# Kernel optimization log

Hardware: AMD Instinct MI355X
Metric: run time of the kernel (lower is better)

## Reference

```python
import jax, jax.numpy as jnp
import numpy as np

EPS = 1e-5  # BatchNorm eps; eval-mode BN with running_mean=0, running_var=1 -> affine


def pe3d(C, x, y, z):
    """PositionalEncoding3D -> (C, x, y, z), faithfully reproducing the torch
    broadcasting (emb_x of shape (x,1,c) assigned into (x,y,z,c) slices)."""
    c = int(np.ceil(C / 3))
    inv_freq = jnp.asarray(1.0 / (10000.0 ** (np.arange(0, c, 2, dtype=np.float32) / c)))
    def emb(n):
        s = jnp.arange(n, dtype=jnp.float32)[:, None] * inv_freq[None, :]
        return jnp.concatenate([jnp.sin(s), jnp.cos(s)], axis=-1)  # (n, c)
    ex = emb(x)[:, None, :]   # (x,1,c) -> broadcasts as (1,x,1,c), same as torch
    ey = emb(y)[:, None, :]   # (y,1,c)
    ez = emb(z)               # (z,c)
    out = jnp.zeros((x, y, z, 3 * c), dtype=jnp.float32)
    out = out.at[..., :c].set(ex)
    out = out.at[..., c:2 * c].set(ey)
    out = out.at[..., 2 * c:3 * c].set(ez)
    return jnp.transpose(out[..., :C], (3, 0, 1, 2))  # (C,x,y,z)


def conv1x1(x, w, b):  # x:(B,Ci,D,H,W) w:(Co,Ci)
    return jnp.einsum('bcdhw,oc->bodhw', x, w) + b[None, :, None, None, None]


def bn_relu(x, g, b):  # eval BN (mean 0, var 1) + ReLU
    s = g / jnp.sqrt(1.0 + EPS)
    return jax.nn.relu(x * s[None, :, None, None, None] + b[None, :, None, None, None])


def setup_inputs() -> dict:
    key = jax.random.key(0)
    ks = jax.random.split(key, 16)
    B, Cy, Cs, D, H, W = 2, 96, 48, 16, 16, 16
    w = lambda k, shp: jax.random.normal(k, shp, dtype=jnp.float32) * 0.05
    return {
        'Y': jax.random.normal(ks[0], (B, Cy, D, H, W), dtype=jnp.float32),
        'S': jax.random.normal(ks[1], (B, Cs, D, H, W), dtype=jnp.float32),
        'w_s': w(ks[2], (Cs, Cs)), 'b_s': jnp.zeros((Cs,), jnp.float32),
        'g_s': jnp.ones((Cs,), jnp.float32), 'be_s': jnp.zeros((Cs,), jnp.float32),
        'w_y': w(ks[3], (Cs, Cy)), 'b_y': jnp.zeros((Cs,), jnp.float32),
        'g_y': jnp.ones((Cs,), jnp.float32), 'be_y': jnp.zeros((Cs,), jnp.float32),
        'Wq': w(ks[4], (Cs, Cs)), 'Wk': w(ks[5], (Cs, Cs)), 'Wv': w(ks[6], (Cs, Cs)),
        'w_o': w(ks[7], (Cs, Cs)), 'b_o': jnp.zeros((Cs,), jnp.float32),
        'g_o': jnp.ones((Cs,), jnp.float32), 'be_o': jnp.zeros((Cs,), jnp.float32),
        'w3': w(ks[8], (Cy, Cy, 3, 3, 3)), 'b3': jnp.zeros((Cy,), jnp.float32),
        'w_y2': w(ks[9], (Cs, Cy)), 'b_y2': jnp.zeros((Cs,), jnp.float32),
        'g_y2': jnp.ones((Cs,), jnp.float32), 'be_y2': jnp.zeros((Cs,), jnp.float32),
    }


def reference(Y, S, w_s, b_s, g_s, be_s, w_y, b_y, g_y, be_y, Wq, Wk, Wv,
              w_o, b_o, g_o, be_o, w3, b3, w_y2, b_y2, g_y2, be_y2):
    B, Cs, D, H, W = S.shape
    Cy = Y.shape[1]
    N = D * H * W
    # positional encodings (added, not learned)
    S = S + pe3d(Cs, D, H, W)[None]
    Y = Y + pe3d(Cy, D, H, W)[None]
    # projections: conv1x1 + BN + ReLU
    S1 = bn_relu(conv1x1(S, w_s, b_s), g_s, be_s).reshape(B, Cs, N).transpose(0, 2, 1)  # (B,N,Cs)
    Y1 = bn_relu(conv1x1(Y, w_y, b_y), g_y, be_y).reshape(B, Cs, N).transpose(0, 2, 1)  # (B,N,Cs)
    # Yconv2: 3x3x3 conv -> 1x1 conv -> BN -> ReLU
    Y3 = jax.lax.conv_general_dilated(Y, w3, (1, 1, 1), 'SAME',
                                      dimension_numbers=('NCDHW', 'OIDHW', 'NCDHW'))
    Y3 = Y3 + b3[None, :, None, None, None]
    Y2 = bn_relu(conv1x1(Y3, w_y2, b_y2), g_y2, be_y2)  # (B,Cs,D,H,W)
    # MultiHeadDense = plain right-matmul by (d,d) weight
    Q = jnp.einsum('bnd,de->bne', Y1, Wq)
    K = jnp.einsum('bnd,de->bne', Y1, Wk)
    V = jnp.einsum('bnd,de->bne', S1, Wv)
    # attention with NON-STANDARD softmax over axis=1 (queries, not keys)
    A = jax.nn.softmax(jnp.einsum('bqd,bkd->bqk', Q, K) * (float(Cs) ** -0.5), axis=1)
    x = jnp.einsum('bqk,bkd->bqd', A, V)                       # (B,N,Cs)
    x = x.transpose(0, 2, 1).reshape(B, Cs, D, H, W)
    Z = bn_relu(conv1x1(x, w_o, b_o), g_o, be_o) * S
    return jnp.concatenate([Z, Y2], axis=1)  # (B, 2*Cs, D, H, W)
```

## Files before the change

### kernel.cpp

```cpp
#include <hip/hip_runtime.h>
#include <hip/hip_bf16.h>

#define NPOS 4096
#define BB 2
#define KS2 32
#define QS2 32

typedef short v4s __attribute__((ext_vector_type(4)));
typedef short v8s __attribute__((ext_vector_type(8)));
typedef float v4f __attribute__((ext_vector_type(4)));
typedef unsigned short ushort_t;

static __device__ __forceinline__ unsigned short f2bf(float f) {
    unsigned int u = __float_as_uint(f);
    return (unsigned short)((u + 0x7fffu + ((u >> 16) & 1u)) >> 16);
}
static __device__ __forceinline__ float bf2f(ushort_t s) {
    return __uint_as_float(((unsigned int)s) << 16);
}

__device__ __forceinline__ float pe_val(int C, int c, int ch, int h, int w) {
    int blk = ch / c;
    int j = ch - blk * c;
    int half = c >> 1;
    int jj = (j < half) ? j : j - half;
    float freq = __expf(-(2.0f * jj / (float)c) * 9.210340371976184f);
    int pos = (blk < 2) ? h : w;
    float s = (float)pos * freq;
    return (j < half) ? __sinf(s) : __cosf(s);
}

__global__ void prep1_kernel(const float* __restrict__ S, const float* __restrict__ Y,
                             const float* __restrict__ w3, float* __restrict__ S_pe,
                             float* __restrict__ Y_pe, ushort_t* __restrict__ wr) {
    int bid = blockIdx.x;
    int t = threadIdx.x;
    __shared__ float tb[16];
    if (bid < 384) {
        int idx4 = bid * 256 + t;
        int ch = (idx4 >> 10) % 48;
        if (t < 16) tb[t] = pe_val(48, 16, ch, t, t);
        __syncthreads();
        int n = (idx4 & 1023) * 4;
        int h = (n >> 4) & 15, w0 = n & 15;
        v4f x = *(const v4f*)&S[(size_t)idx4 * 4];
        if (ch < 32) {
            float p = tb[h];
#pragma unroll
            for (int j = 0; j < 4; j++) x[j] += p;
        } else {
#pragma unroll
            for (int j = 0; j < 4; j++) x[j] += tb[w0 + j];
        }
        *(v4f*)&S_pe[(size_t)idx4 * 4] = x;
    } else if (bid < 1152) {
        int idx4 = (bid - 384) * 256 + t;
        int ch = (idx4 >> 10) % 96;
        if (t < 16) tb[t] = pe_val(96, 32, ch, t, t);
        __syncthreads();
        int n = (idx4 & 1023) * 4;
        int h = (n >> 4) & 15, w0 = n & 15;
        v4f x = *(const v4f*)&Y[(size_t)idx4 * 4];
        if (ch < 64) {
            float p = tb[h];
#pragma unroll
            for (int j = 0; j < 4; j++) x[j] += p;
        } else {
#pragma unroll
            for (int j = 0; j < 4; j++) x[j] += tb[w0 + j];
        }
        *(v4f*)&Y_pe[(size_t)idx4 * 4] = x;
    } else {
        int idx = (bid - 1152) * 256 + t;
        if (idx < 27 * 96 * 96) {
            int ci = idx % 96;
            int t2 = idx / 96;
            int co = t2 % 96;
            int tap = t2 / 96;
            wr[idx] = f2bf(w3[(size_t)(co * 96 + ci) * 27 + tap]);
        }
    }
}

template<int CI>
__device__ __forceinline__ void proj_body(int r, const float* __restrict__ in,
                                          const float* __restrict__ w, const float* __restrict__ bias,
                                          const float* __restrict__ g, const float* __restrict__ be,
                                          float* __restrict__ out) {
    int pc = r >> 3, cc = r & 7;
    int o0 = cc * 6;
    __shared__ float wl[6 * CI];
    __shared__ float sb[6], bb[6];
    int t = threadIdx.x;
    for (int i = t; i < 6 * CI; i += 256) {
        int o = i / CI, ci = i - o * CI;
        wl[i] = w[(size_t)(o0 + o) * CI + ci];
    }
    if (t < 6) {
        float s = g[o0 + t] * rsqrtf(1.0f + 1e-5f);
        sb[t] = s; bb[t] = bias[o0 + t] * s + be[o0 + t];
    }
    __syncthreads();
    int gn = pc * 256 + t;
    int b = gn >> 12;
    const float* ip = in + (size_t)b * CI * NPOS + (gn & 4095);
    float acc[6];
#pragma unroll
    for (int o = 0; o < 6; o++) acc[o] = 0.f;
#pragma unroll
    for (int ci = 0; ci < CI; ci++) {
        float v = ip[(size_t)ci * NPOS];
#pragma unroll
        for (int o = 0; o < 6; o++) acc[o] += v * wl[o * CI + ci];
    }
    float* op = out + (size_t)gn * 48 + o0;
#pragma unroll
    for (int o = 0; o < 6; o++) {
        float z = acc[o] * sb[o] + bb[o];
        op[o] = z > 0.f ? z : 0.f;
    }
}

__global__ void prep2_kernel(const float* __restrict__ Y_pe, const float* __restrict__ S_pe,
                             const float* __restrict__ w_s, const float* __restrict__ b_s,
                             const float* __restrict__ g_s, const float* __restrict__ be_s,
                             const float* __restrict__ w_y, const float* __restrict__ b_y,
                             const float* __restrict__ g_y, const float* __restrict__ be_y,
                             ushort_t* __restrict__ Ypad, float* __restrict__ S1,
                             float* __restrict__ Y1) {
    int bid = blockIdx.x;
    if (bid < 1094) {
        int idx = bid * 256 + threadIdx.x;
        if (idx >= BB * 5832 * 24) return;
        int ci4 = idx % 24;
        int cell = idx / 24;
        int wp = cell % 18; int c2 = cell / 18;
        int hp = c2 % 18; int c3 = c2 / 18;
        int zp = c3 % 18; int b = c3 / 18;
        ushort_t pk[4] = {0, 0, 0, 0};
        if (zp >= 1 && zp <= 16 && hp >= 1 && hp <= 16 && wp >= 1 && wp <= 16) {
            int n = (zp - 1) * 256 + (hp - 1) * 16 + (wp - 1);
#pragma unroll
            for (int j = 0; j < 4; j++)
                pk[j] = f2bf(Y_pe[((size_t)(b * 96 + ci4 * 4 + j) << 12) + n]);
        }
        *(v4s*)&Ypad[(size_t)idx * 4] = *(v4s*)pk;
    } else {
        int r = bid - 1094;
        if (r < 256) proj_body<48>(r, S_pe, w_s, b_s, g_s, be_s, S1);
        else proj_body<96>(r - 256, Y_pe, w_y, b_y, g_y, be_y, Y1);
    }
}

__global__ void qkv_kernel(const float* __restrict__ Y1, const float* __restrict__ S1,
                           const float* __restrict__ Wq, const float* __restrict__ Wk,
                           const float* __restrict__ Wv, ushort_t* __restrict__ Qb,
                           ushort_t* __restrict__ Kb, ushort_t* __restrict__ Vt) {
    int grp = blockIdx.x >> 8;
    int r = blockIdx.x & 255;
    int pc = r >> 3, cc = r & 7;
    int o0 = cc * 6;
    const float* in = (grp == 2) ? S1 : Y1;
    const float* w = (grp == 0) ? Wq : (grp == 1) ? Wk : Wv;
    __shared__ float wl[48 * 6];
    int t = threadIdx.x;
    for (int i = t; i < 48 * 6; i += 256) {
        int d = i / 6, o = i - d * 6;
        wl[i] = w[(size_t)d * 48 + o0 + o];
    }
    __syncthreads();
    int gn = pc * 256 + t;
    const float* ip = in + (size_t)gn * 48;
    float acc[6];
#pragma unroll
    for (int o = 0; o < 6; o++) acc[o] = 0.f;
#pragma unroll
    for (int d = 0; d < 48; d++) {
        float v = ip[d];
#pragma unroll
        for (int o = 0; o < 6; o++) acc[o] += v * wl[d * 6 + o];
    }
    if (grp < 2) {
        ushort_t* base = (grp == 0 ? Qb : Kb) + (size_t)gn * 64;
#pragma unroll
        for (int o = 0; o < 6; o++) base[o0 + o] = f2bf(acc[o]);
        if (cc == 0) {
            v8s z = {0, 0, 0, 0, 0, 0, 0, 0};
            *(v8s*)(base + 48) = z;
            *(v8s*)(base + 56) = z;
        }
    } else {
        int b = gn >> 12; int n = gn & 4095;
#pragma unroll
        for (int o = 0; o < 6; o++)
            Vt[((size_t)(b * 48 + o0 + o) << 12) + n] = f2bf(acc[o]);
    }
}

__global__ void attn_stats_mfma_kernel(const ushort_t* __restrict__ Qb,
                                       const ushort_t* __restrict__ Kb,
                                       float* __restrict__ ps) {
    int bid = blockIdx.x;
    int qs = bid & 31; int kb = (bid >> 5) & 15; int b = bid >> 9;
    int t = threadIdx.x; int wv = t >> 6; int lane = t & 63;
    int lr = lane & 15, g = lane >> 4;
    const float scale = 0.14433756729740643f;
    int key0 = kb * 256 + wv * 64;
    v8s ka[4][2];
#pragma unroll
    for (int kt = 0; kt < 4; kt++) {
        const ushort_t* krow = Kb + ((size_t)(b * NPOS + key0 + kt * 16 + lr)) * 64;
        ka[kt][0] = *(const v8s*)(krow + 8 * g);
        ka[kt][1] = *(const v8s*)(krow + 32 + 8 * g);
    }
    float s[4][4];
#pragma unroll
    for (int kt = 0; kt < 4; kt++)
#pragma unroll
        for (int r = 0; r < 4; r++) s[kt][r] = 0.f;
    for (int qt = 0; qt < 8; qt++) {
        int q = qs * 128 + qt * 16 + lr;
        const ushort_t* qrow = Qb + ((size_t)(b * NPOS + q)) * 64;
        v8s qf0 = *(const v8s*)(qrow + 8 * g);
        v8s qf1 = *(const v8s*)(qrow + 32 + 8 * g);
#pragma unroll
        for (int kt = 0; kt < 4; kt++) {
            v4f acc = {0.f, 0.f, 0.f, 0.f};
            acc = __builtin_amdgcn_mfma_f32_16x16x32_bf16(ka[kt][0], qf0, acc, 0, 0, 0);
            acc = __builtin_amdgcn_mfma_f32_16x16x32_bf16(ka[kt][1], qf1, acc, 0, 0, 0);
#pragma unroll
            for (int r = 0; r < 4; r++) s[kt][r] += __expf(acc[r] * scale);
        }
    }
#pragma unroll
    for (int off = 1; off < 16; off <<= 1)
#pragma unroll
        for (int kt = 0; kt < 4; kt++)
#pragma unroll
            for (int r = 0; r < 4; r++) s[kt][r] += __shfl_xor(s[kt][r], off);
    if (lr == 0) {
#pragma unroll
        for (int kt = 0; kt < 4; kt++) {
            int idx = (b * QS2 + qs) * NPOS + key0 + kt * 16 + 4 * g;
            v4f ss = {s[kt][0], s[kt][1], s[kt][2], s[kt][3]};
            *(v4f*)&ps[idx] = ss;
        }
    }
}

__global__ void norm_vscale_kernel(const float* __restrict__ ps, ushort_t* __restrict__ Vt) {
    int idx = blockIdx.x * 256 + threadIdx.x;
    if (idx >= BB * 4 * NPOS) return;
    int k = idx & 4095;
    int rest = idx >> 12;
    int dg = rest & 3; int b = rest >> 2;
    float s = 0.f;
#pragma unroll
    for (int qs = 0; qs < QS2; qs++) s += ps[(size_t)(b * QS2 + qs) * NPOS + k];
    float ci = 1.0f / s;
#pragma unroll
    for (int d = dg * 12; d < dg * 12 + 12; d++) {
        size_t a = ((size_t)(b * 48 + d) << 12) + k;
        Vt[a] = f2bf(bf2f(Vt[a]) * ci);
    }
}

__device__ __forceinline__ void pv_body(int bid, const ushort_t* __restrict__ Qb,
                                        const ushort_t* __restrict__ Kb,
                                        const ushort_t* __restrict__ Vt,
                                        ushort_t* __restrict__ xpart) {
    __shared__ ushort_t Kl[128 * 64];
    __shared__ ushort_t Vl[48 * 128];
    int ks = bid & 31; int qb = (bid >> 5) & 15; int b = bid >> 9;
    int t = threadIdx.x; int wv = t >> 6; int lane = t & 63;
    int lr = lane & 15, g = lane >> 4;
    const float scale = 0.14433756729740643f;
    int kb0 = ks * 128;
    {
        const ushort_t* src = Kb + ((size_t)(b * NPOS + kb0)) * 64;
        for (int i = t; i < 1024; i += 256) {
            int row = i >> 3, slot = i & 7;
            *(v8s*)&Kl[row * 64 + ((slot ^ (row & 7)) << 3)] =
                *(const v8s*)(src + row * 64 + slot * 8);
        }
        const ushort_t* vsrc = Vt + ((size_t)(b * 48) << 12) + kb0;
        for (int i = t; i < 1536; i += 256) {
            int row = i >> 5, s8 = i & 31;
            *(v4s*)&Vl[row * 128 + ((s8 ^ (row & 15)) << 2)] =
                *(const v4s*)(vsrc + ((size_t)row << 12) + s8 * 4);
        }
    }
    int q0 = qb * 256 + wv * 64;
    v8s qf[4][2];
#pragma unroll
    for (int qt = 0; qt < 4; qt++) {
        const ushort_t* qrow = Qb + ((size_t)(b * NPOS + q0 + qt * 16 + lr)) * 64;
        qf[qt][0] = *(const v8s*)(qrow + 8 * g);
        qf[qt][1] = *(const v8s*)(qrow + 32 + 8 * g);
    }
    __syncthreads();
    v4f xacc[4][3];
#pragma unroll
    for (int qt = 0; qt < 4; qt++)
#pragma unroll
        for (int nt = 0; nt < 3; nt++) xacc[qt][nt] = (v4f){0.f, 0.f, 0.f, 0.f};
    for (int kt = 0; kt < 2; kt++) {
        v4s p[4][4];
#pragma unroll
        for (int tm = 0; tm < 4; tm++) {
            int krow = kt * 64 + 16 * tm + lr;
            v8s ka0 = *(const v8s*)&Kl[krow * 64 + ((g ^ (krow & 7)) << 3)];
            v8s ka1 = *(const v8s*)&Kl[krow * 64 + (((4 + g) ^ (krow & 7)) << 3)];
#pragma unroll
            for (int qt = 0; qt < 4; qt++) {
                v4f acc = {0.f, 0.f, 0.f, 0.f};
                acc = __builtin_amdgcn_mfma_f32_16x16x32_bf16(ka0, qf[qt][0], acc, 0, 0, 0);
                acc = __builtin_amdgcn_mfma_f32_16x16x32_bf16(ka1, qf[qt][1], acc, 0, 0, 0);
                v4s pp;
#pragma unroll
                for (int r = 0; r < 4; r++)
                    pp[r] = (short)f2bf(__expf(acc[r] * scale));
                p[tm][qt] = pp;
            }
        }
#pragma unroll
        for (int nt = 0; nt < 3; nt++) {
#pragma unroll
            for (int tm = 0; tm < 4; tm++) {
                int vrowd = 16 * nt + lr;
                int s8 = 16 * kt + 4 * tm + g;
                v4s vf = *(const v4s*)&Vl[vrowd * 128 + ((s8 ^ (vrowd & 15)) << 2)];
#pragma unroll
                for (int qt = 0; qt < 4; qt++)
                    xacc[qt][nt] = __builtin_amdgcn_mfma_f32_16x16x16bf16_1k(
                        p[tm][qt], vf, xacc[qt][nt], 0, 0, 0);
            }
        }
    }
#pragma unroll
    for (int qt = 0; qt < 4; qt++)
#pragma unroll
        for (int nt = 0; nt < 3; nt++)
#pragma unroll
            for (int r = 0; r < 4; r++)
                xpart[(((size_t)(b * KS2 + ks) << 12) + q0 + qt * 16 + 4 * g + r) * 48 + 16 * nt + lr] =
                    f2bf(xacc[qt][nt][r]);
}

__device__ __forceinline__ void conv_body(int bid, const ushort_t* __restrict__ Ypad,
                                          const ushort_t* __restrict__ wr,
                                          const float* __restrict__ b3,
                                          float* __restrict__ Y3) {
    int b = bid / 384;
    int r = bid % 384;
    int cot = r % 6;
    int zhq = r / 6;
    int t = threadIdx.x; int wv = t >> 6; int lane = t & 63;
    int z = zhq >> 2;
    int h = (zhq & 3) * 4 + wv;
    int lr = lane & 15, g = lane >> 4;
    v4f acc[3];
#pragma unroll
    for (int kd = 0; kd < 3; kd++) acc[kd] = (v4f){0.f, 0.f, 0.f, 0.f};
    const ushort_t* wbase = wr + (size_t)(cot * 16 + lr) * 96 + 8 * g;
#pragma unroll
    for (int kd = 0; kd < 3; kd++) {
#pragma unroll
        for (int kh = 0; kh < 3; kh++) {
            const ushort_t* arow = Ypad + (((size_t)(b * 18 + z + kd) * 18 + h + kh) * 18 + lr) * 96 + 8 * g;
            int tap0 = (kd * 3 + kh) * 3;
            v8s af[3][3], bf[3][3];
#pragma unroll
            for (int kw = 0; kw < 3; kw++)
#pragma unroll
                for (int c = 0; c < 3; c++) {
                    af[kw][c] = *(const v8s*)(arow + kw * 96 + c * 32);
                    bf[kw][c] = *(const v8s*)(wbase + (size_t)(tap0 + kw) * 96 * 96 + c * 32);
                }
#pragma unroll
            for (int kw = 0; kw < 3; kw++)
#pragma unroll
                for (int c = 0; c < 3; c++)
                    acc[kd] = __builtin_amdgcn_mfma_f32_16x16x32_bf16(
                        af[kw][c], bf[kw][c], acc[kd], 0, 0, 0);
        }
    }
    float bv = b3[cot * 16 + lr];
    int pos = z * 256 + h * 16 + 4 * g;
#pragma unroll
    for (int r2 = 0; r2 < 4; r2++)
        Y3[(((size_t)b << 12) + pos + r2) * 96 + cot * 16 + lr] =
            acc[0][r2] + acc[1][r2] + acc[2][r2] + bv;
}

__global__ __launch_bounds__(256, 2)
void pvconv_kernel(const ushort_t* __restrict__ Qb, const ushort_t* __restrict__ Kb,
                   const ushort_t* __restrict__ Vt, ushort_t* __restrict__ xpart,
                   const ushort_t* __restrict__ Ypad, const ushort_t* __restrict__ wr,
                   const float* __restrict__ b3, float* __restrict__ Y3) {
    int g7 = blockIdx.x / 7, r7 = blockIdx.x % 7;
    if (r7 < 4) pv_body(g7 * 4 + r7, Qb, Kb, Vt, xpart);
    else conv_body(g7 * 3 + (r7 - 4), Ypad, wr, b3, Y3);
}

__global__ void xreduce_kernel(const ushort_t* __restrict__ xpart, float* __restrict__ xsum) {
    int v = blockIdx.x * 256 + threadIdx.x;
    if (v >= BB * NPOS * 6) return;
    int b = v / (NPOS * 6);
    int rem8 = (v - b * NPOS * 6) * 8;
    float s[8];
#pragma unroll
    for (int j = 0; j < 8; j++) s[j] = 0.f;
    const ushort_t* base = xpart + (size_t)b * KS2 * NPOS * 48 + rem8;
#pragma unroll 4
    for (int ks = 0; ks < KS2; ks++) {
        v8s x = *(const v8s*)(base + (size_t)ks * NPOS * 48);
#pragma unroll
        for (int j = 0; j < 8; j++) s[j] += bf2f((ushort_t)x[j]);
    }
    float* op = xsum + (size_t)b * NPOS * 48 + rem8;
    v4f lo = {s[0], s[1], s[2], s[3]};
    v4f hi = {s[4], s[5], s[6], s[7]};
    *(v4f*)op = lo;
    *(v4f*)(op + 4) = hi;
}

__device__ __forceinline__ void z_out_body(int r, const float* __restrict__ xsum,
                                           const float* __restrict__ w_o, const float* __restrict__ b_o,
                                           const float* __restrict__ g_o, const float* __restrict__ be_o,
                                           const float* __restrict__ S_pe, float* __restrict__ out) {
    int pc = r >> 3, cc = r & 7;
    int o0 = cc * 6;
    __shared__ float wl[6 * 48];
    __shared__ float sb[6], bb[6];
    int t = threadIdx.x;
    for (int i = t; i < 6 * 48; i += 256) {
        int o = i / 48, d = i - o * 48;
        wl[i] = w_o[(size_t)(o0 + o) * 48 + d];
    }
    if (t < 6) {
        float s = g_o[o0 + t] * rsqrtf(1.f + 1e-5f);
        sb[t] = s; bb[t] = b_o[o0 + t] * s + be_o[o0 + t];
    }
    __syncthreads();
    int gn = pc * 256 + t;
    int b = gn >> 12; int n = gn & 4095;
    const v4f* p = (const v4f*)(xsum + (size_t)gn * 48);
    float x[48];
#pragma unroll
    for (int d4 = 0; d4 < 12; d4++) {
        v4f v = p[d4];
#pragma unroll
        for (int j = 0; j < 4; j++) x[d4 * 4 + j] = v[j];
    }
#pragma unroll
    for (int o = 0; o < 6; o++) {
        float acc = 0.f;
#pragma unroll
        for (int d = 0; d < 48; d++) acc += wl[o * 48 + d] * x[d];
        float z = acc * sb[o] + bb[o];
        z = z > 0.f ? z : 0.f;
        out[((size_t)b * 96 + o0 + o) * NPOS + n] = z * S_pe[((size_t)b * 48 + o0 + o) * NPOS + n];
    }
}

__device__ __forceinline__ void y2_out_body(int r, const float* __restrict__ Y3,
                                            const float* __restrict__ w_y2, const float* __restrict__ b_y2,
                                            const float* __restrict__ g_y2, const float* __restrict__ be_y2,
                                            float* __restrict__ out) {
    int pc = r >> 3, cc = r & 7;
    int o0 = cc * 6;
    __shared__ float wl2[6 * 96];
    __shared__ float sb2[6], bb2[6];
    int t = threadIdx.x;
    for (int i = t; i < 6 * 96; i += 256) {
        int o = i / 96, ci = i - o * 96;
        wl2[i] = w_y2[(size_t)(o0 + o) * 96 + ci];
    }
    if (t < 6) {
        float s = g_y2[o0 + t] * rsqrtf(1.f + 1e-5f);
        sb2[t] = s; bb2[t] = b_y2[o0 + t] * s + be_y2[o0 + t];
    }
    __syncthreads();
    int gn = pc * 256 + t;
    int b = gn >> 12; int n = gn & 4095;
    const v4f* ip = (const v4f*)(Y3 + (size_t)gn * 96);
    float acc[6];
#pragma unroll
    for (int o = 0; o < 6; o++) acc[o] = 0.f;
#pragma unroll
    for (int c4 = 0; c4 < 24; c4++) {
        v4f v = ip[c4];
#pragma unroll
        for (int j = 0; j < 4; j++)
#pragma unroll
            for (int o = 0; o < 6; o++) acc[o] += v[j] * wl2[o * 96 + c4 * 4 + j];
    }
#pragma unroll
    for (int o = 0; o < 6; o++) {
        float z = acc[o] * sb2[o] + bb2[o];
        out[((size_t)b * 96 + 48 + o0 + o) * NPOS + n] = z > 0.f ? z : 0.f;
    }
}

__global__ void zy_out_kernel(const float* __restrict__ xsum, const float* __restrict__ w_o,
                              const float* __restrict__ b_o, const float* __restrict__ g_o,
                              const float* __restrict__ be_o, const float* __restrict__ S_pe,
                              const float* __restrict__ Y3, const float* __restrict__ w_y2,
                              const float* __restrict__ b_y2, const float* __restrict__ g_y2,
                              const float* __restrict__ be_y2, float* __restrict__ out) {
    int bid = blockIdx.x;
    if (bid < 256) z_out_body(bid, xsum, w_o, b_o, g_o, be_o, S_pe, out);
    else y2_out_body(bid - 256, Y3, w_y2, b_y2, g_y2, be_y2, out);
}

extern "C" void kernel_launch(void* const* d_in, const int* in_sizes, int n_in,
                              void* d_out, int out_size, void* d_ws, size_t ws_size,
                              hipStream_t stream) {
    const float* Y    = (const float*)d_in[0];
    const float* S    = (const float*)d_in[1];
    const float* w_s  = (const float*)d_in[2];
    const float* b_s  = (const float*)d_in[3];
    const float* g_s  = (const float*)d_in[4];
    const float* be_s = (const float*)d_in[5];
    const float* w_y  = (const float*)d_in[6];
    const float* b_y  = (const float*)d_in[7];
    const float* g_y  = (const float*)d_in[8];
    const float* be_y = (const float*)d_in[9];
    const float* Wq   = (const float*)d_in[10];
    const float* Wk   = (const float*)d_in[11];
    const float* Wv   = (const float*)d_in[12];
    const float* w_o  = (const float*)d_in[13];
    const float* b_o  = (const float*)d_in[14];
    const float* g_o  = (const float*)d_in[15];
    const float* be_o = (const float*)d_in[16];
    const float* w3   = (const float*)d_in[17];
    const float* b3   = (const float*)d_in[18];
    const float* w_y2 = (const float*)d_in[19];
    const float* b_y2 = (const float*)d_in[20];
    const float* g_y2 = (const float*)d_in[21];
    const float* be_y2= (const float*)d_in[22];
    float* out = (float*)d_out;

    float* ws = (float*)d_ws;
    float* S_pe   = ws;
    float* Y_pe   = ws + 393216;
    float* S1     = ws + 1179648;
    float* Y1     = ws + 1572864;
    ushort_t* Qb  = (ushort_t*)(ws + 1966080);
    ushort_t* Kb  = (ushort_t*)(ws + 2228224);
    ushort_t* Vt  = (ushort_t*)(ws + 2490368);
    float* ps     = ws + 2686976;
    ushort_t* xpart = (ushort_t*)(ws + 2949120);
    float* xsum   = ws + 9240576;
    float* Y3     = ws + 9633792;
    ushort_t* Ypad= (ushort_t*)(ws + 10420224);
    ushort_t* wr  = (ushort_t*)(ws + 10980096);

    prep1_kernel<<<2124, 256, 0, stream>>>(S, Y, w3, S_pe, Y_pe, wr);
    prep2_kernel<<<1606, 256, 0, stream>>>(Y_pe, S_pe, w_s, b_s, g_s, be_s,
                                           w_y, b_y, g_y, be_y, Ypad, S1, Y1);
    qkv_kernel<<<768, 256, 0, stream>>>(Y1, S1, Wq, Wk, Wv, Qb, Kb, Vt);
    attn_stats_mfma_kernel<<<BB * 16 * QS2, 256, 0, stream>>>(Qb, Kb, ps);
    norm_vscale_kernel<<<128, 256, 0, stream>>>(ps, Vt);
    pvconv_kernel<<<BB * 16 * KS2 + 768, 256, 0, stream>>>(Qb, Kb, Vt, xpart,
                                                           Ypad, wr, b3, Y3);
    xreduce_kernel<<<192, 256, 0, stream>>>(xpart, xsum);
    zy_out_kernel<<<512, 256, 0, stream>>>(xsum, w_o, b_o, g_o, be_o, S_pe,
                                           Y3, w_y2, b_y2, g_y2, be_y2, out);
}
```

Before: 133.9 us.

## Fold positional encoding into consumers and fuse softmax column norm into PV

Removes the standalone PE-add pass that materialised S_pe and Y_pe. The encoding is now recomputed from small shared-memory tables inside the pad, projection and output kernels, which merge the two prep launches into one. The separate normalisation kernel that rescaled V by the column sums is dropped; each PV block now sums the partial stats for its keys and multiplies the exponentials by the reciprocal. Each PV block also covers 256 keys in two tiles (KS2 halved), which shrinks the partial buffer and the reduction but adds redundant ps reads and an extra sync per block.

Result: no change. 136.2 us (+1.8%).

```diff
diff --git a/kernel.cpp b/kernel.cpp
--- a/kernel.cpp
+++ b/kernel.cpp
@@ -3,7 +3,7 @@
 
 #define NPOS 4096
 #define BB 2
-#define KS2 32
+#define KS2 16
 #define QS2 32
 
 typedef short v4s __attribute__((ext_vector_type(4)));
@@ -30,59 +30,34 @@
     return (j < half) ? __sinf(s) : __cosf(s);
 }
 
-__global__ void prep1_kernel(const float* __restrict__ S, const float* __restrict__ Y,
-                             const float* __restrict__ w3, float* __restrict__ S_pe,
-                             float* __restrict__ Y_pe, ushort_t* __restrict__ wr) {
-    int bid = blockIdx.x;
+__device__ __forceinline__ void pad_body(int r, const float* __restrict__ Y,
+                                         ushort_t* __restrict__ Ypad) {
+    __shared__ float tb[96 * 16];
     int t = threadIdx.x;
-    __shared__ float tb[16];
-    if (bid < 384) {
-        int idx4 = bid * 256 + t;
-        int ch = (idx4 >> 10) % 48;
-        if (t < 16) tb[t] = pe_val(48, 16, ch, t, t);
-        __syncthreads();
-        int n = (idx4 & 1023) * 4;
-        int h = (n >> 4) & 15, w0 = n & 15;
-        v4f x = *(const v4f*)&S[(size_t)idx4 * 4];
-        if (ch < 32) {
-            float p = tb[h];
-#pragma unroll
-            for (int j = 0; j < 4; j++) x[j] += p;
-        } else {
-#pragma unroll
-            for (int j = 0; j < 4; j++) x[j] += tb[w0 + j];
-        }
-        *(v4f*)&S_pe[(size_t)idx4 * 4] = x;
-    } else if (bid < 1152) {
-        int idx4 = (bid - 384) * 256 + t;
-        int ch = (idx4 >> 10) % 96;
-        if (t < 16) tb[t] = pe_val(96, 32, ch, t, t);
-        __syncthreads();
-        int n = (idx4 & 1023) * 4;
-        int h = (n >> 4) & 15, w0 = n & 15;
-        v4f x = *(const v4f*)&Y[(size_t)idx4 * 4];
-        if (ch < 64) {
-            float p = tb[h];
-#pragma unroll
-            for (int j = 0; j < 4; j++) x[j] += p;
-        } else {
-#pragma unroll
-            for (int j = 0; j < 4; j++) x[j] += tb[w0 + j];
-        }
-        *(v4f*)&Y_pe[(size_t)idx4 * 4] = x;
-    } else {
-        int idx = (bid - 1152) * 256 + t;
-        if (idx < 27 * 96 * 96) {
-            int ci = idx % 96;
-            int t2 = idx / 96;
-            int co = t2 % 96;
-            int tap = t2 / 96;
-            wr[idx] = f2bf(w3[(size_t)(co * 96 + ci) * 27 + tap]);
-        }
-    }
-}
-
-template<int CI>
+    for (int i = t; i < 96 * 16; i += 256) tb[i] = pe_val(96, 32, i >> 4, i & 15, i & 15);
+    __syncthreads();
+    int idx = r * 256 + t;
+    if (idx >= BB * 5832 * 24) return;
+    int ci4 = idx % 24;
+    int cell = idx / 24;
+    int wp = cell % 18; int c2 = cell / 18;
+    int hp = c2 % 18; int c3 = c2 / 18;
+    int zp = c3 % 18; int b = c3 / 18;
+    ushort_t pk[4] = {0, 0, 0, 0};
+    if (zp >= 1 && zp <= 16 && hp >= 1 && hp <= 16 && wp >= 1 && wp <= 16) {
+        int n = (zp - 1) * 256 + (hp - 1) * 16 + (wp - 1);
+        int h = hp - 1, w0 = wp - 1;
+#pragma unroll
+        for (int j = 0; j < 4; j++) {
+            int ch = ci4 * 4 + j;
+            float pe = tb[ch * 16 + (ch < 64 ? h : w0)];
+            pk[j] = f2bf(Y[((size_t)(b * 96 + ch) << 12) + n] + pe);
+        }
+    }
+    *(v4s*)&Ypad[(size_t)idx * 4] = *(v4s*)pk;
+}
+
+template<int CI, int CC>
 __device__ __forceinline__ void proj_body(int r, const float* __restrict__ in,
                                           const float* __restrict__ w, const float* __restrict__ bias,
                                           const float* __restrict__ g, const float* __restrict__ be,
@@ -90,12 +65,14 @@
     int pc = r >> 3, cc = r & 7;
     int o0 = cc * 6;
     __shared__ float wl[6 * CI];
+    __shared__ float tb[CI * 16];
     __shared__ float sb[6], bb[6];
     int t = threadIdx.x;
     for (int i = t; i < 6 * CI; i += 256) {
         int o = i / CI, ci = i - o * CI;
         wl[i] = w[(size_t)(o0 + o) * CI + ci];
     }
+    for (int i = t; i < CI * 16; i += 256) tb[i] = pe_val(CI, CC, i >> 4, i & 15, i & 15);
     if (t < 6) {
         float s = g[o0 + t] * rsqrtf(1.0f + 1e-5f);
         sb[t] = s; bb[t] = bias[o0 + t] * s + be[o0 + t];
@@ -103,13 +80,15 @@
     __syncthreads();
     int gn = pc * 256 + t;
     int b = gn >> 12;
-    const float* ip = in + (size_t)b * CI * NPOS + (gn & 4095);
+    int n = gn & 4095;
+    int h = (n >> 4) & 15, w0 = n & 15;
+    const float* ip = in + (size_t)b * CI * NPOS + n;
     float acc[6];
 #pragma unroll
     for (int o = 0; o < 6; o++) acc[o] = 0.f;
 #pragma unroll
     for (int ci = 0; ci < CI; ci++) {
-        float v = ip[(size_t)ci * NPOS];
+        float v = ip[(size_t)ci * NPOS] + tb[ci * 16 + (ci < 2 * CC ? h : w0)];
 #pragma unroll
         for (int o = 0; o < 6; o++) acc[o] += v * wl[o * CI + ci];
     }
@@ -121,34 +100,30 @@
     }
 }
 
-__global__ void prep2_kernel(const float* __restrict__ Y_pe, const float* __restrict__ S_pe,
-                             const float* __restrict__ w_s, const float* __restrict__ b_s,
-                             const float* __restrict__ g_s, const float* __restrict__ be_s,
-                             const float* __restrict__ w_y, const float* __restrict__ b_y,
-                             const float* __restrict__ g_y, const float* __restrict__ be_y,
-                             ushort_t* __restrict__ Ypad, float* __restrict__ S1,
-                             float* __restrict__ Y1) {
+__global__ void prep_kernel(const float* __restrict__ S, const float* __restrict__ Y,
+                            const float* __restrict__ w3,
+                            const float* __restrict__ w_s, const float* __restrict__ b_s,
+                            const float* __restrict__ g_s, const float* __restrict__ be_s,
+                            const float* __restrict__ w_y, const float* __restrict__ b_y,
+                            const float* __restrict__ g_y, const float* __restrict__ be_y,
+                            ushort_t* __restrict__ Ypad, float* __restrict__ S1,
+                            float* __restrict__ Y1, ushort_t* __restrict__ wr) {
     int bid = blockIdx.x;
     if (bid < 1094) {
-        int idx = bid * 256 + threadIdx.x;
-        if (idx >= BB * 5832 * 24) return;
-        int ci4 = idx % 24;
-        int cell = idx / 24;
-        int wp = cell % 18; int c2 = cell / 18;
-        int hp = c2 % 18; int c3 = c2 / 18;
-        int zp = c3 % 18; int b = c3 / 18;
-        ushort_t pk[4] = {0, 0, 0, 0};
-        if (zp >= 1 && zp <= 16 && hp >= 1 && hp <= 16 && wp >= 1 && wp <= 16) {
-            int n = (zp - 1) * 256 + (hp - 1) * 16 + (wp - 1);
-#pragma unroll
-            for (int j = 0; j < 4; j++)
-                pk[j] = f2bf(Y_pe[((size_t)(b * 96 + ci4 * 4 + j) << 12) + n]);
-        }
-        *(v4s*)&Ypad[(size_t)idx * 4] = *(v4s*)pk;
+        pad_body(bid, Y, Ypad);
+    } else if (bid < 1350) {
+        proj_body<48, 16>(bid - 1094, S, w_s, b_s, g_s, be_s, S1);
+    } else if (bid < 1606) {
+        proj_body<96, 32>(bid - 1350, Y, w_y, b_y, g_y, be_y, Y1);
     } else {
-        int r = bid - 1094;
-        if (r < 256) proj_body<48>(r, S_pe, w_s, b_s, g_s, be_s, S1);
-        else proj_body<96>(r - 256, Y_pe, w_y, b_y, g_y, be_y, Y1);
+        int idx = (bid - 1606) * 256 + threadIdx.x;
+        if (idx < 27 * 96 * 96) {
+            int ci = idx % 96;
+            int t2 = idx / 96;
+            int co = t2 % 96;
+            int tap = t2 / 96;
+            wr[idx] = f2bf(w3[(size_t)(co * 96 + ci) * 27 + tap]);
+        }
     }
 }
 
@@ -248,48 +223,18 @@
     }
 }
 
-__global__ void norm_vscale_kernel(const float* __restrict__ ps, ushort_t* __restrict__ Vt) {
-    int idx = blockIdx.x * 256 + threadIdx.x;
-    if (idx >= BB * 4 * NPOS) return;
-    int k = idx & 4095;
-    int rest = idx >> 12;
-    int dg = rest & 3; int b = rest >> 2;
-    float s = 0.f;
-#pragma unroll
-    for (int qs = 0; qs < QS2; qs++) s += ps[(size_t)(b * QS2 + qs) * NPOS + k];
-    float ci = 1.0f / s;
-#pragma unroll
-    for (int d = dg * 12; d < dg * 12 + 12; d++) {
-        size_t a = ((size_t)(b * 48 + d) << 12) + k;
-        Vt[a] = f2bf(bf2f(Vt[a]) * ci);
-    }
-}
-
 __device__ __forceinline__ void pv_body(int bid, const ushort_t* __restrict__ Qb,
                                         const ushort_t* __restrict__ Kb,
                                         const ushort_t* __restrict__ Vt,
+                                        const float* __restrict__ ps,
                                         ushort_t* __restrict__ xpart) {
     __shared__ ushort_t Kl[128 * 64];
     __shared__ ushort_t Vl[48 * 128];
-    int ks = bid & 31; int qb = (bid >> 5) & 15; int b = bid >> 9;
+    __shared__ float ciL[128];
+    int ks = bid & 15; int qb = (bid >> 4) & 15; int b = bid >> 8;
     int t = threadIdx.x; int wv = t >> 6; int lane = t & 63;
     int lr = lane & 15, g = lane >> 4;
     const float scale = 0.14433756729740643f;
-    int kb0 = ks * 128;
-    {
-        const ushort_t* src = Kb + ((size_t)(b * NPOS + kb0)) * 64;
-        for (int i = t; i < 1024; i += 256) {
-            int row = i >> 3, slot = i & 7;
-            *(v8s*)&Kl[row * 64 + ((slot ^ (row & 7)) << 3)] =
-                *(const v8s*)(src + row * 64 + slot * 8);
-        }
-        const ushort_t* vsrc = Vt + ((size_t)(b * 48) << 12) + kb0;
-        for (int i = t; i < 1536; i += 256) {
-            int row = i >> 5, s8 = i & 31;
-            *(v4s*)&Vl[row * 128 + ((s8 ^ (row & 15)) << 2)] =
-                *(const v4s*)(vsrc + ((size_t)row << 12) + s8 * 4);
-        }
-    }
     int q0 = qb * 256 + wv * 64;
     v8s qf[4][2];
 #pragma unroll
@@ -298,42 +243,68 @@
         qf[qt][0] = *(const v8s*)(qrow + 8 * g);
         qf[qt][1] = *(const v8s*)(qrow + 32 + 8 * g);
     }
-    __syncthreads();
     v4f xacc[4][3];
 #pragma unroll
     for (int qt = 0; qt < 4; qt++)
 #pragma unroll
         for (int nt = 0; nt < 3; nt++) xacc[qt][nt] = (v4f){0.f, 0.f, 0.f, 0.f};
-    for (int kt = 0; kt < 2; kt++) {
-        v4s p[4][4];
-#pragma unroll
-        for (int tm = 0; tm < 4; tm++) {
-            int krow = kt * 64 + 16 * tm + lr;
-            v8s ka0 = *(const v8s*)&Kl[krow * 64 + ((g ^ (krow & 7)) << 3)];
-            v8s ka1 = *(const v8s*)&Kl[krow * 64 + (((4 + g) ^ (krow & 7)) << 3)];
-#pragma unroll
-            for (int qt = 0; qt < 4; qt++) {
-                v4f acc = {0.f, 0.f, 0.f, 0.f};
-                acc = __builtin_amdgcn_mfma_f32_16x16x32_bf16(ka0, qf[qt][0], acc, 0, 0, 0);
-                acc = __builtin_amdgcn_mfma_f32_16x16x32_bf16(ka1, qf[qt][1], acc, 0, 0, 0);
-                v4s pp;
-#pragma unroll
-                for (int r = 0; r < 4; r++)
-                    pp[r] = (short)f2bf(__expf(acc[r] * scale));
-                p[tm][qt] = pp;
+    for (int tile = 0; tile < 2; tile++) {
+        int kb0 = ks * 256 + tile * 128;
+        if (tile) __syncthreads();
+        {
+            const ushort_t* src = Kb + ((size_t)(b * NPOS + kb0)) * 64;
+            for (int i = t; i < 1024; i += 256) {
+                int row = i >> 3, slot = i & 7;
+                *(v8s*)&Kl[row * 64 + ((slot ^ (row & 7)) << 3)] =
+                    *(const v8s*)(src + row * 64 + slot * 8);
             }
-        }
-#pragma unroll
-        for (int nt = 0; nt < 3; nt++) {
+            const ushort_t* vsrc = Vt + ((size_t)(b * 48) << 12) + kb0;
+            for (int i = t; i < 1536; i += 256) {
+                int row = i >> 5, s8 = i & 31;
+                *(v4s*)&Vl[row * 128 + ((s8 ^ (row & 15)) << 2)] =
+                    *(const v4s*)(vsrc + ((size_t)row << 12) + s8 * 4);
+            }
+            if (t < 128) {
+                float s = 0.f;
+#pragma unroll
+                for (int qs = 0; qs < QS2; qs++)
+                    s += ps[(size_t)(b * QS2 + qs) * NPOS + kb0 + t];
+                ciL[t] = 1.0f / s;
+            }
+        }
+        __syncthreads();
+        for (int kt = 0; kt < 2; kt++) {
+            v4s p[4][4];
 #pragma unroll
             for (int tm = 0; tm < 4; tm++) {
-                int vrowd = 16 * nt + lr;
-                int s8 = 16 * kt + 4 * tm + g;
-                v4s vf = *(const v4s*)&Vl[vrowd * 128 + ((s8 ^ (vrowd & 15)) << 2)];
-#pragma unroll
-                for (int qt = 0; qt < 4; qt++)
-                    xacc[qt][nt] = __builtin_amdgcn_mfma_f32_16x16x16bf16_1k(
-                        p[tm][qt], vf, xacc[qt][nt], 0, 0, 0);
+                int krow = kt * 64 + 16 * tm + lr;
+                v8s ka0 = *(const v8s*)&Kl[krow * 64 + ((g ^ (krow & 7)) << 3)];
+                v8s ka1 = *(const v8s*)&Kl[krow * 64 + (((4 + g) ^ (krow & 7)) << 3)];
+                v4f ci = *(const v4f*)&ciL[kt * 64 + 16 * tm + 4 * g];
+#pragma unroll
+                for (int qt = 0; qt < 4; qt++) {
+                    v4f acc = {0.f, 0.f, 0.f, 0.f};
+                    acc = __builtin_amdgcn_mfma_f32_16x16x32_bf16(ka0, qf[qt][0], acc, 0, 0, 0);
+                    acc = __builtin_amdgcn_mfma_f32_16x16x32_bf16(ka1, qf[qt][1], acc, 0, 0, 0);
+                    v4s pp;
+#pragma unroll
+                    for (int r = 0; r < 4; r++)
+                        pp[r] = (short)f2bf(__expf(acc[r] * scale) * ci[r]);
+                    p[tm][qt] = pp;
+                }
+            }
+#pragma unroll
+            for (int nt = 0; nt < 3; nt++) {
+#pragma unroll
+                for (int tm = 0; tm < 4; tm++) {
+                    int vrowd = 16 * nt + lr;
+                    int s8 = 16 * kt + 4 * tm + g;
+                    v4s vf = *(const v4s*)&Vl[vrowd * 128 + ((s8 ^ (vrowd & 15)) << 2)];
+#pragma unroll
+                    for (int qt = 0; qt < 4; qt++)
+                        xacc[qt][nt] = __builtin_amdgcn_mfma_f32_16x16x16bf16_1k(
+                            p[tm][qt], vf, xacc[qt][nt], 0, 0, 0);
+                }
             }
         }
     }
@@ -395,12 +366,13 @@
 
 __global__ __launch_bounds__(256, 2)
 void pvconv_kernel(const ushort_t* __restrict__ Qb, const ushort_t* __restrict__ Kb,
-                   const ushort_t* __restrict__ Vt, ushort_t* __restrict__ xpart,
+                   const ushort_t* __restrict__ Vt, const float* __restrict__ ps,
+                   ushort_t* __restrict__ xpart,
                    const ushort_t* __restrict__ Ypad, const ushort_t* __restrict__ wr,
                    const float* __restrict__ b3, float* __restrict__ Y3) {
-    int g7 = blockIdx.x / 7, r7 = blockIdx.x % 7;
-    if (r7 < 4) pv_body(g7 * 4 + r7, Qb, Kb, Vt, xpart);
-    else conv_body(g7 * 3 + (r7 - 4), Ypad, wr, b3, Y3);
+    int g5 = blockIdx.x / 5, r5 = blockIdx.x % 5;
+    if (r5 < 2) pv_body(g5 * 2 + r5, Qb, Kb, Vt, ps, xpart);
+    else conv_body(g5 * 3 + (r5 - 2), Ypad, wr, b3, Y3);
 }
 
 __global__ void xreduce_kernel(const ushort_t* __restrict__ xpart, float* __restrict__ xsum) {
@@ -428,16 +400,18 @@
 __device__ __forceinline__ void z_out_body(int r, const float* __restrict__ xsum,
                                            const float* __restrict__ w_o, const float* __restrict__ b_o,
                                            const float* __restrict__ g_o, const float* __restrict__ be_o,
-                                           const float* __restrict__ S_pe, float* __restrict__ out) {
+                                           const float* __restrict__ S, float* __restrict__ out) {
     int pc = r >> 3, cc = r & 7;
     int o0 = cc * 6;
     __shared__ float wl[6 * 48];
+    __shared__ float tbz[6 * 16];
     __shared__ float sb[6], bb[6];
     int t = threadIdx.x;
     for (int i = t; i < 6 * 48; i += 256) {
         int o = i / 48, d = i - o * 48;
         wl[i] = w_o[(size_t)(o0 + o) * 48 + d];
     }
+    if (t < 96) tbz[t] = pe_val(48, 16, o0 + t / 16, t & 15, t & 15);
     if (t < 6) {
         float s = g_o[o0 + t] * rsqrtf(1.f + 1e-5f);
         sb[t] = s; bb[t] = b_o[o0 + t] * s + be_o[o0 + t];
@@ -445,6 +419,7 @@
     __syncthreads();
     int gn = pc * 256 + t;
     int b = gn >> 12; int n = gn & 4095;
+    int h = (n >> 4) & 15, w0 = n & 15;
     const v4f* p = (const v4f*)(xsum + (size_t)gn * 48);
     float x[48];
 #pragma unroll
@@ -460,7 +435,9 @@
         for (int d = 0; d < 48; d++) acc += wl[o * 48 + d] * x[d];
         float z = acc * sb[o] + bb[o];
         z = z > 0.f ? z : 0.f;
-        out[((size_t)b * 96 + o0 + o) * NPOS + n] = z * S_pe[((size_t)b * 48 + o0 + o) * NPOS + n];
+        float spe = S[((size_t)b * 48 + o0 + o) * NPOS + n] +
+                    tbz[o * 16 + (o0 + o < 32 ? h : w0)];
+        out[((size_t)b * 96 + o0 + o) * NPOS + n] = z * spe;
     }
 }
 
@@ -505,12 +482,12 @@
 
 __global__ void zy_out_kernel(const float* __restrict__ xsum, const float* __restrict__ w_o,
                               const float* __restrict__ b_o, const float* __restrict__ g_o,
-                              const float* __restrict__ be_o, const float* __restrict__ S_pe,
+                              const float* __restrict__ be_o, const float* __restrict__ S,
                               const float* __restrict__ Y3, const float* __restrict__ w_y2,
                               const float* __restrict__ b_y2, const float* __restrict__ g_y2,
                               const float* __restrict__ be_y2, float* __restrict__ out) {
     int bid = blockIdx.x;
-    if (bid < 256) z_out_body(bid, xsum, w_o, b_o, g_o, be_o, S_pe, out);
+    if (bid < 256) z_out_body(bid, xsum, w_o, b_o, g_o, be_o, S, out);
     else y2_out_body(bid - 256, Y3, w_y2, b_y2, g_y2, be_y2, out);
 }
 
@@ -543,29 +520,24 @@
     float* out = (float*)d_out;
 
     float* ws = (float*)d_ws;
-    float* S_pe   = ws;
-    float* Y_pe   = ws + 393216;
-    float* S1     = ws + 1179648;
-    float* Y1     = ws + 1572864;
-    ushort_t* Qb  = (ushort_t*)(ws + 1966080);
-    ushort_t* Kb  = (ushort_t*)(ws + 2228224);
-    ushort_t* Vt  = (ushort_t*)(ws + 2490368);
-    float* ps     = ws + 2686976;
-    ushort_t* xpart = (ushort_t*)(ws + 2949120);
-    float* xsum   = ws + 9240576;
-    float* Y3     = ws + 9633792;
-    ushort_t* Ypad= (ushort_t*)(ws + 10420224);
-    ushort_t* wr  = (ushort_t*)(ws + 10980096);
-
-    prep1_kernel<<<2124, 256, 0, stream>>>(S, Y, w3, S_pe, Y_pe, wr);
-    prep2_kernel<<<1606, 256, 0, stream>>>(Y_pe, S_pe, w_s, b_s, g_s, be_s,
-                                           w_y, b_y, g_y, be_y, Ypad, S1, Y1);
+    float* S1     = ws;
+    float* Y1     = ws + 393216;
+    ushort_t* Qb  = (ushort_t*)(ws + 786432);
+    ushort_t* Kb  = (ushort_t*)(ws + 1048576);
+    ushort_t* Vt  = (ushort_t*)(ws + 1310720);
+    float* ps     = ws + 1507328;
+    ushort_t* xpart = (ushort_t*)(ws + 1769472);
+    float* xsum   = ws + 4915200;
+    float* Y3     = ws + 5308416;
+    ushort_t* Ypad= (ushort_t*)(ws + 6094848);
+    ushort_t* wr  = (ushort_t*)(ws + 6654720);
+
+    prep_kernel<<<2578, 256, 0, stream>>>(S, Y, w3, w_s, b_s, g_s, be_s,
+                                          w_y, b_y, g_y, be_y, Ypad, S1, Y1, wr);
     qkv_kernel<<<768, 256, 0, stream>>>(Y1, S1, Wq, Wk, Wv, Qb, Kb, Vt);
     attn_stats_mfma_kernel<<<BB * 16 * QS2, 256, 0, stream>>>(Qb, Kb, ps);
-    norm_vscale_kernel<<<128, 256, 0, stream>>>(ps, Vt);
-    pvconv_kernel<<<BB * 16 * KS2 + 768, 256, 0, stream>>>(Qb, Kb, Vt, xpart,
-                                                           Ypad, wr, b3, Y3);
+    pvconv_kernel<<<1280, 256, 0, stream>>>(Qb, Kb, Vt, ps, xpart, Ypad, wr, b3, Y3);
     xreduce_kernel<<<192, 256, 0, stream>>>(xpart, xsum);
-    zy_out_kernel<<<512, 256, 0, stream>>>(xsum, w_o, b_o, g_o, be_o, S_pe,
+    zy_out_kernel<<<512, 256, 0, stream>>>(xsum, w_o, b_o, g_o, be_o, S,
                                            Y3, w_y2, b_y2, g_y2, be_y2, out);
 }
```
